# Kernel optimization log

Measured on AMD Instinct MI355X. Metric: run time of the kernel, lower is better.

Reference implementation:

```python
import jax, jax.numpy as jnp
import numpy as np

B, N, C, H, W = 4, 64, 256, 64, 64
ROI = 7          # roi_samples
S = 3            # ceil(16px / 7) sample points per ROI cell (boxes fixed at 16px)
HALF = 0.125     # fixed normalized half-size -> 16px boxes on 64-grid -> static S
N_INT = ROI * S  # interpolation grid side length (21)


def setup_inputs() -> dict:
    key = jax.random.key(0)
    k1, k2, k3, k4, k5 = jax.random.split(key, 5)
    img = jax.random.normal(k1, (B, C, H, W), jnp.float32)
    cen = jax.random.uniform(k2, (B, N, 2), jnp.float32, minval=0.2, maxval=0.8)
    # boxes_bn22 = [(x1,y1),(x2,y2)], normalized coords, fixed size so that
    # custom_roi_align's ceil(box_px/roi) == S for every box
    boxes = jnp.stack([cen - HALF, cen + HALF], axis=2)  # (B,N,2,2)
    conv_w = jax.random.normal(k3, (C, C, ROI, ROI), jnp.float32) * 0.02
    conv_b = jnp.zeros((C,), jnp.float32)
    cxcywh_w = jax.random.normal(k4, (C, 4), jnp.float32) * 0.02
    cxcywh_b = jnp.zeros((C,), jnp.float32)
    posenc_w = jax.random.normal(k5, (C, C + 2), jnp.float32) * 0.02
    posenc_b = jnp.zeros((C,), jnp.float32)
    return {"image_tokens_bchw": img, "boxes_bn22": boxes,
            "conv_w": conv_w, "conv_b": conv_b,
            "cxcywh_w": cxcywh_w, "cxcywh_b": cxcywh_b,
            "posenc_w": posenc_w, "posenc_b": posenc_b}


def _pe_1d(coord, num_feats):
    # DETR/SAM-style sinusoidal PE of a scalar coordinate -> (n, num_feats)
    dim_t = 10000.0 ** (2.0 * (jnp.arange(num_feats) // 2) / num_feats)
    pos = coord[:, None] * (2.0 * jnp.pi) / dim_t.astype(coord.dtype)
    enc = jnp.stack([jnp.sin(pos[:, 0::2]), jnp.cos(pos[:, 1::2])], axis=-1)
    return enc.reshape(coord.shape[0], num_feats)


def _roi_align(img_bchw, boxes_f4, bidx):
    # Faithful vectorization of custom_roi_align: per-box uniform sample grid,
    # bilinear grid_sample (align_corners=True, border pad), then SxS avg-pool.
    nsx = W / (W - 1.0)
    nsy = H / (H - 1.0)
    t = jnp.arange(N_INT, dtype=img_bchw.dtype) / (N_INT - 1)

    def one(b, box):
        x1, y1, x2, y2 = box[0] * nsx, box[1] * nsy, box[2] * nsx, box[3] * nsy
        hsx = (x2 - x1) / (2 * N_INT)
        hsy = (y2 - y1) / (2 * N_INT)
        gx = (x1 + hsx) + t * (x2 - x1 - 2 * hsx)  # linspace over box interior
        gy = (y1 + hsy) + t * (y2 - y1 - 2 * hsy)
        # align_corners=True pixel coords; border padding == clamp
        px = jnp.clip(gx * (W - 1), 0.0, W - 1.0)
        py = jnp.clip(gy * (H - 1), 0.0, H - 1.0)
        x0f, y0f = jnp.floor(px), jnp.floor(py)
        wx, wy = px - x0f, py - y0f
        x0 = jnp.clip(x0f.astype(jnp.int32), 0, W - 1)
        x1i = jnp.clip(x0 + 1, 0, W - 1)
        y0 = jnp.clip(y0f.astype(jnp.int32), 0, H - 1)
        y1i = jnp.clip(y0 + 1, 0, H - 1)
        img = img_bchw[b]                               # (C,H,W)
        v00 = img[:, y0[:, None], x0[None, :]]          # (C,N_INT,N_INT)
        v01 = img[:, y0[:, None], x1i[None, :]]
        v10 = img[:, y1i[:, None], x0[None, :]]
        v11 = img[:, y1i[:, None], x1i[None, :]]
        top = v00 + (v01 - v00) * wx[None, None, :]
        bot = v10 + (v11 - v10) * wx[None, None, :]
        samp = top + (bot - top) * wy[None, :, None]    # (C,N_INT,N_INT)
        # avg_pool2d with kernel (S,S) stride (S,S)
        return samp.reshape(C, ROI, S, ROI, S).mean(axis=(2, 4))  # (C,ROI,ROI)

    return jax.vmap(one)(bidx, boxes_f4)


def reference(image_tokens_bchw, boxes_bn22, conv_w, conv_b,
              cxcywh_w, cxcywh_b, posenc_w, posenc_b):
    boxes_f4 = boxes_bn22.reshape(B * N, 4)
    bidx = jnp.repeat(jnp.arange(B), N)
    roi = _roi_align(image_tokens_bchw, boxes_f4, bidx)      # (BN,C,ROI,ROI)
    # 7x7 conv over a 7x7 map -> 1x1: a plain contraction
    img_enc = (jnp.einsum('nchw,ochw->no', roi, conv_w) + conv_b).reshape(B, N, C)

    cen = boxes_bn22.mean(axis=2)                            # (B,N,2) cx,cy
    wh = boxes_bn22[:, :, 1] - boxes_bn22[:, :, 0]           # (B,N,2) w,h
    cxcywh = jnp.concatenate([cen, wh], axis=-1)             # (B,N,4)
    flat = cxcywh.reshape(B * N, 4)
    x_enc = _pe_1d(flat[:, 0], C // 2)
    y_enc = _pe_1d(flat[:, 1], C // 2)
    pe_tok = jnp.concatenate([y_enc, x_enc, flat[:, 3:4], flat[:, 2:3]], axis=-1)
    pos_enc = (pe_tok @ posenc_w.T + posenc_b).reshape(B, N, C)
    base = cxcywh @ cxcywh_w.T + cxcywh_b                    # (B,N,C)
    return base + pos_enc + img_enc
```

## Files before the change

### kernel.cpp

```cpp
#include <hip/hip_runtime.h>

static constexpr int KDIM = 12544;
static constexpr float TWO_PI = 6.28318530717958647692f;

typedef float f32x4 __attribute__((ext_vector_type(4)));
typedef short bf16x8 __attribute__((ext_vector_type(8)));

__device__ inline float bf2f(unsigned short u) {
    union { unsigned int i; float f; } x; x.i = ((unsigned int)u) << 16; return x.f;
}
__device__ inline unsigned short f2bf(float f) {
    union { float f; unsigned int i; } x; x.f = f;
    unsigned int r = (x.i + 0x7FFFu + ((x.i >> 16) & 1u)) >> 16;
    return (unsigned short)r;
}

__global__ __launch_bounds__(256) void k_prep(
    const float* __restrict__ boxes,
    const float* __restrict__ cxw, const float* __restrict__ cxb,
    const float* __restrict__ pw,  const float* __restrict__ pb,
    const float* __restrict__ cb,
    const float* __restrict__ img, const float* __restrict__ convw,
    float* __restrict__ out,
    unsigned short* __restrict__ imgT, unsigned short* __restrict__ Wt,
    float4* __restrict__ lutx, float4* __restrict__ luty)
{
    __shared__ float smem[12544];
    const int bid = blockIdx.x;
    const int tid = threadIdx.x;

    if (bid < 256) {
        const int n = bid;
        const float bx1 = boxes[n*4+0], by1 = boxes[n*4+1];
        const float bx2 = boxes[n*4+2], by2 = boxes[n*4+3];
        const float cx = 0.5f*(bx1+bx2), cy = 0.5f*(by1+by2);
        const float wx = bx2-bx1,        wy = by2-by1;

        float* pe = smem;

        if (tid < 128) {
            const int   k     = tid & 63;
            const float coord = (tid < 64) ? cy : cx;
            const float d   = exp2f((float)k * (13.287712379549449f / 64.0f));
            const float arg = coord * TWO_PI / d;
            float s, c;
            sincosf(arg, &s, &c);
            const int base = (tid < 64) ? 0 : 128;
            pe[base + 2*k]     = s;
            pe[base + 2*k + 1] = c;
        } else if (tid == 128) {
            pe[256] = wy;
            pe[257] = wx;
        } else if (tid >= 160 && tid < 202) {
            const int  t   = tid - 160;
            const bool isx = (t < 21);
            const int  i   = isx ? t : (t - 21);
            const float ns = 64.0f / 63.0f;
            const float a1 = (isx ? bx1 : by1) * ns;
            const float a2 = (isx ? bx2 : by2) * ns;
            const float hs = (a2 - a1) * (1.0f / 42.0f);
            const float tt = (float)i * (1.0f / 20.0f);
            const float g  = a1 + hs + tt * (a2 - a1 - 2.0f*hs);
            float p = g * 63.0f;
            p = fminf(fmaxf(p, 0.0f), 63.0f);
            const float p0 = floorf(p);
            const float w  = p - p0;
            int i0 = (int)p0; i0 = min(i0, 63);
            const int i1 = min(i0 + 1, 63);
            (isx ? lutx : luty)[n*21 + i] = make_float4((float)i0, (float)i1, w, 0.0f);
        }
        __syncthreads();

        const int o = tid;
        float acc = pb[o] + cb[o] + cxb[o];
        acc = fmaf(cxw[o*4+0], cx, acc);
        acc = fmaf(cxw[o*4+1], cy, acc);
        acc = fmaf(cxw[o*4+2], wx, acc);
        acc = fmaf(cxw[o*4+3], wy, acc);
        const float* __restrict__ pwr = pw + o*258;
        for (int k = 0; k < 258; ++k)
            acc = fmaf(pe[k], pwr[k], acc);
        out[n*256 + o] = acc;
    } else if (bid < 1280) {
        float (*t)[65] = (float(*)[65])smem;
        const int idx = bid - 256;
        const int b   = idx >> 8;
        const int rem = idx & 255;
        const int c0  = (rem & 3) * 64;
        const int p0  = (rem >> 2) * 64;
        const int col = tid & 63;
        const int r4  = tid >> 6;
        #pragma unroll
        for (int i = 0; i < 16; ++i) {
            const int row = i*4 + r4;
            t[row][col] = img[((size_t)(b*256 + c0 + row)) * 4096 + p0 + col];
        }
        __syncthreads();
        #pragma unroll
        for (int i = 0; i < 16; ++i) {
            const int prow = i*4 + r4;
            imgT[((size_t)(b*4096 + p0 + prow)) * 256 + c0 + col] = f2bf(t[col][prow]);
        }
    } else {
        const int o = bid - 1280;
        #pragma unroll
        for (int i = 0; i < 49; ++i)
            smem[i*256 + tid] = convw[(size_t)o*12544 + i*256 + tid];
        __syncthreads();
        for (int ij = 0; ij < 49; ++ij)
            Wt[(size_t)o*12544 + ij*256 + tid] = f2bf(smem[tid*49 + ij]);
    }
}

__global__ __launch_bounds__(256) void k_fused(
    const unsigned short* __restrict__ imgT,
    const unsigned short* __restrict__ Wt,
    const float4* __restrict__ lutx, const float4* __restrict__ luty,
    float* __restrict__ out)
{
    __shared__ __align__(16) char ldsA[8192];
    __shared__ __align__(16) char ldsW[32768];

    const int mt = blockIdx.x;
    const int ij = blockIdx.y;
    const int m0 = mt * 16;
    const int pi = ij / 7, pj = ij - pi * 7;
    const int tid = threadIdx.x;
    const int w = tid >> 6, l = tid & 63;
    const int l15 = l & 15, lg = l >> 4;
    const int c4 = l * 4;

    for (int bi = 0; bi < 4; ++bi) {
        const int r = w * 4 + bi;
        const int n = m0 + r;
        const int b = n >> 6;
        const unsigned short* __restrict__ base = imgT + ((size_t)b << 20) + c4;

        const float4 lx0 = lutx[n*21 + pj*3 + 0];
        const float4 lx1 = lutx[n*21 + pj*3 + 1];
        const float4 lx2 = lutx[n*21 + pj*3 + 2];

        float a0 = 0.f, a1 = 0.f, a2 = 0.f, a3 = 0.f;
        #pragma unroll
        for (int si = 0; si < 3; ++si) {
            const float4 ly = luty[n*21 + pi*3 + si];
            const unsigned short* __restrict__ r0 = base + (((int)ly.x) << 14);
            const unsigned short* __restrict__ r1 = base + (((int)ly.y) << 14);
            const float wyy = ly.z;
            const float4 lxs[3] = {lx0, lx1, lx2};
            #pragma unroll
            for (int sj = 0; sj < 3; ++sj) {
                const float4 lx = lxs[sj];
                const int x0 = ((int)lx.x) << 8, x1 = ((int)lx.y) << 8;
                const float wxx = lx.z;
                const ushort4 v00 = *(const ushort4*)(r0 + x0);
                const ushort4 v01 = *(const ushort4*)(r0 + x1);
                const ushort4 v10 = *(const ushort4*)(r1 + x0);
                const ushort4 v11 = *(const ushort4*)(r1 + x1);
                {
                    const float t = fmaf(bf2f(v01.x) - bf2f(v00.x), wxx, bf2f(v00.x));
                    const float u = fmaf(bf2f(v11.x) - bf2f(v10.x), wxx, bf2f(v10.x));
                    a0 += fmaf(u - t, wyy, t);
                }
                {
                    const float t = fmaf(bf2f(v01.y) - bf2f(v00.y), wxx, bf2f(v00.y));
                    const float u = fmaf(bf2f(v11.y) - bf2f(v10.y), wxx, bf2f(v10.y));
                    a1 += fmaf(u - t, wyy, t);
                }
                {
                    const float t = fmaf(bf2f(v01.z) - bf2f(v00.z), wxx, bf2f(v00.z));
                    const float u = fmaf(bf2f(v11.z) - bf2f(v10.z), wxx, bf2f(v10.z));
                    a2 += fmaf(u - t, wyy, t);
                }
                {
                    const float t = fmaf(bf2f(v01.w) - bf2f(v00.w), wxx, bf2f(v00.w));
                    const float u = fmaf(bf2f(v11.w) - bf2f(v10.w), wxx, bf2f(v10.w));
                    a3 += fmaf(u - t, wyy, t);
                }
            }
        }
        const float s = 1.0f / 9.0f;
        ushort4 o4;
        o4.x = f2bf(a0 * s); o4.y = f2bf(a1 * s);
        o4.z = f2bf(a2 * s); o4.w = f2bf(a3 * s);
        *(ushort4*)&ldsA[(r * 512 + l * 8) ^ ((r & 7) << 4)] = o4;
    }
    __syncthreads();

    const int bcol = w * 16 + l15;
    #pragma unroll 1
    for (int oc = 0; oc < 4; ++oc) {
        if (oc) __syncthreads();
        #pragma unroll
        for (int it = 0; it < 8; ++it) {
            const int chunk = tid + it * 256;
            const int row = chunk >> 5, ci = chunk & 31;
            *(float4*)&ldsW[(row * 512 + ci * 16) ^ ((row & 7) << 4)] =
                *(const float4*)(Wt + (size_t)(oc * 64 + row) * KDIM + ij * 256 + ci * 8);
        }
        __syncthreads();

        f32x4 acc = {};
        #pragma unroll
        for (int ks = 0; ks < 8; ++ks) {
            const int koff = ks * 64 + lg * 16;
            const bf16x8 bfrag =
                *(const bf16x8*)&ldsW[(bcol * 512 + koff) ^ ((bcol & 7) << 4)];
            const bf16x8 afrag =
                *(const bf16x8*)&ldsA[(l15 * 512 + koff) ^ ((l15 & 7) << 4)];
            acc = __builtin_amdgcn_mfma_f32_16x16x32_bf16(afrag, bfrag, acc, 0, 0, 0);
        }
        #pragma unroll
        for (int j = 0; j < 4; ++j)
            unsafeAtomicAdd(&out[(m0 + lg * 4 + j) * 256 + oc * 64 + bcol], acc[j]);
    }
}

extern "C" void kernel_launch(void* const* d_in, const int* in_sizes, int n_in,
                              void* d_out, int out_size, void* d_ws, size_t ws_size,
                              hipStream_t stream)
{
    const float* img   = (const float*)d_in[0];
    const float* boxes = (const float*)d_in[1];
    const float* convw = (const float*)d_in[2];
    const float* convb = (const float*)d_in[3];
    const float* cxw   = (const float*)d_in[4];
    const float* cxb   = (const float*)d_in[5];
    const float* pw    = (const float*)d_in[6];
    const float* pb    = (const float*)d_in[7];
    float* out = (float*)d_out;

    unsigned short* imgT = (unsigned short*)d_ws;
    unsigned short* Wt   = (unsigned short*)((char*)d_ws + 8388608);
    float4*         lutx = (float4*)((char*)d_ws + 14811136);
    float4*         luty = (float4*)((char*)d_ws + 14897152);

    k_prep<<<1536, 256, 0, stream>>>(boxes, cxw, cxb, pw, pb, convb,
                                     img, convw, out, imgT, Wt, lutx, luty);
    k_fused<<<dim3(16, 49), 256, 0, stream>>>(imgT, Wt, lutx, luty, out);
}
```

Baseline: 128.4 us.

## Prefetch weights via direct global-to-LDS loads, remap blocks per XCD, split weight transpose

In the fused kernel the first weight tile is now fetched straight into shared memory with global_load_lds, issued before the bilinear sampling so the fetch overlaps that work. The XOR swizzle moves from the LDS address to the global source address. The 1D grid is remapped so blocks on the same XCD share a batch image, which should improve L2 locality for imgT. The conv-weight transpose in the prep kernel is split into four blocks per output channel with a smaller padded LDS tile, which raises occupancy and parallelism for the prep kernel.

Measured after the change: 130.3 us. No clear change (+1.5%).

```diff
diff --git a/kernel.cpp b/kernel.cpp
--- a/kernel.cpp
+++ b/kernel.cpp
@@ -14,6 +14,11 @@
     unsigned int r = (x.i + 0x7FFFu + ((x.i >> 16) & 1u)) >> 16;
     return (unsigned short)r;
 }
+
+#define GLOAD_LDS16(g, s)                                                          \
+    __builtin_amdgcn_global_load_lds(                                              \
+        (const __attribute__((address_space(1))) unsigned int*)(g),                \
+        (__attribute__((address_space(3))) unsigned int*)(s), 16, 0, 0)
 
 __global__ __launch_bounds__(256) void k_prep(
     const float* __restrict__ boxes,
@@ -25,7 +30,7 @@
     unsigned short* __restrict__ imgT, unsigned short* __restrict__ Wt,
     float4* __restrict__ lutx, float4* __restrict__ luty)
 {
-    __shared__ float smem[12544];
+    __shared__ float smem[64 * 65];
     const int bid = blockIdx.x;
     const int tid = threadIdx.x;
 
@@ -102,13 +107,29 @@
             imgT[((size_t)(b*4096 + p0 + prow)) * 256 + c0 + col] = f2bf(t[col][prow]);
         }
     } else {
-        const int o = bid - 1280;
-        #pragma unroll
-        for (int i = 0; i < 49; ++i)
-            smem[i*256 + tid] = convw[(size_t)o*12544 + i*256 + tid];
+        const int cidx = bid - 1280;
+        const int o    = cidx >> 2;
+        const int c0   = (cidx & 3) << 6;
+        float* cw_t = smem;
+        #pragma unroll
+        for (int it = 0; it < 13; ++it) {
+            const int idx = tid + it * 256;
+            if (idx < 3136) {
+                const int row = idx / 49;
+                const int col = idx - row * 49;
+                cw_t[row * 53 + col] =
+                    convw[(size_t)o * 12544 + (size_t)(c0 + row) * 49 + col];
+            }
+        }
         __syncthreads();
-        for (int ij = 0; ij < 49; ++ij)
-            Wt[(size_t)o*12544 + ij*256 + tid] = f2bf(smem[tid*49 + ij]);
+        const int lane = tid & 63, grp = tid >> 6;
+        #pragma unroll
+        for (int ijg = 0; ijg < 13; ++ijg) {
+            const int ij = grp * 13 + ijg;
+            if (ij < 49)
+                Wt[(size_t)o * 12544 + ij * 256 + c0 + lane] =
+                    f2bf(cw_t[lane * 53 + ij]);
+        }
     }
 }
 
@@ -121,20 +142,31 @@
     __shared__ __align__(16) char ldsA[8192];
     __shared__ __align__(16) char ldsW[32768];
 
-    const int mt = blockIdx.x;
-    const int ij = blockIdx.y;
-    const int m0 = mt * 16;
+    const int bid = blockIdx.x;
+    const int xcd = bid & 7;
+    const int bb  = xcd >> 1;
+    const int j   = bid >> 3;
+    const int ij  = j >> 1;
+    const int mtb = (xcd & 1) + ((j & 1) << 1);
+    const int n0  = bb * 64 + mtb * 16;
     const int pi = ij / 7, pj = ij - pi * 7;
     const int tid = threadIdx.x;
     const int w = tid >> 6, l = tid & 63;
     const int l15 = l & 15, lg = l >> 4;
     const int c4 = l * 4;
 
+    #pragma unroll
+    for (int it = 0; it < 8; ++it) {
+        const int chunk = tid + it * 256;
+        const int row = chunk >> 5, ci = chunk & 31;
+        GLOAD_LDS16(Wt + (size_t)row * KDIM + ij * 256 + ((ci ^ (row & 7)) << 3),
+                    ldsW + chunk * 16);
+    }
+
+    const unsigned short* __restrict__ base = imgT + ((size_t)bb << 20) + c4;
     for (int bi = 0; bi < 4; ++bi) {
         const int r = w * 4 + bi;
-        const int n = m0 + r;
-        const int b = n >> 6;
-        const unsigned short* __restrict__ base = imgT + ((size_t)b << 20) + c4;
+        const int n = n0 + r;
 
         const float4 lx0 = lutx[n*21 + pj*3 + 0];
         const float4 lx1 = lutx[n*21 + pj*3 + 1];
@@ -190,16 +222,18 @@
     const int bcol = w * 16 + l15;
     #pragma unroll 1
     for (int oc = 0; oc < 4; ++oc) {
-        if (oc) __syncthreads();
-        #pragma unroll
-        for (int it = 0; it < 8; ++it) {
-            const int chunk = tid + it * 256;
-            const int row = chunk >> 5, ci = chunk & 31;
-            *(float4*)&ldsW[(row * 512 + ci * 16) ^ ((row & 7) << 4)] =
-                *(const float4*)(Wt + (size_t)(oc * 64 + row) * KDIM + ij * 256 + ci * 8);
-        }
-        __syncthreads();
-
+        if (oc) {
+            __syncthreads();
+            #pragma unroll
+            for (int it = 0; it < 8; ++it) {
+                const int chunk = tid + it * 256;
+                const int row = chunk >> 5, ci = chunk & 31;
+                GLOAD_LDS16(Wt + (size_t)(oc * 64 + row) * KDIM + ij * 256
+                               + ((ci ^ (row & 7)) << 3),
+                            ldsW + chunk * 16);
+            }
+            __syncthreads();
+        }
         f32x4 acc = {};
         #pragma unroll
         for (int ks = 0; ks < 8; ++ks) {
@@ -211,8 +245,8 @@
             acc = __builtin_amdgcn_mfma_f32_16x16x32_bf16(afrag, bfrag, acc, 0, 0, 0);
         }
         #pragma unroll
-        for (int j = 0; j < 4; ++j)
-            unsafeAtomicAdd(&out[(m0 + lg * 4 + j) * 256 + oc * 64 + bcol], acc[j]);
+        for (int jj = 0; jj < 4; ++jj)
+            unsafeAtomicAdd(&out[(n0 + lg * 4 + jj) * 256 + oc * 64 + bcol], acc[jj]);
     }
 }
 
@@ -235,7 +269,7 @@
     float4*         lutx = (float4*)((char*)d_ws + 14811136);
     float4*         luty = (float4*)((char*)d_ws + 14897152);
 
-    k_prep<<<1536, 256, 0, stream>>>(boxes, cxw, cxb, pw, pb, convb,
+    k_prep<<<2304, 256, 0, stream>>>(boxes, cxw, cxb, pw, pb, convb,
                                      img, convw, out, imgT, Wt, lutx, luty);
-    k_fused<<<dim3(16, 49), 256, 0, stream>>>(imgT, Wt, lutx, luty, out);
-}
+    k_fused<<<784, 256, 0, stream>>>(imgT, Wt, lutx, luty, out);
+}
```
